# Kernel optimization log

Measured on AMD Instinct MI355X. Metric: run time of the kernel, lower is better.

The kernel has to match this reference:

```python
import jax, jax.numpy as jnp
import numpy as np

N, M, D = 1024, 1024, 256

def setup_inputs() -> dict:
    key = jax.random.key(0)
    ks = jax.random.split(key, 10)
    s = 1.0 / np.sqrt(D)
    return {
        "f_r": jax.random.normal(ks[0], (N, D), jnp.float32),
        "f_r_prime": jax.random.normal(ks[1], (M, D), jnp.float32),
        "W_w": jax.random.uniform(ks[2], (D, D), jnp.float32, -s, s),
        "W_b": jax.random.uniform(ks[3], (D,), jnp.float32, -s, s),
        "Wp_w": jax.random.uniform(ks[4], (D, D), jnp.float32, -s, s),
        "Wp_b": jax.random.uniform(ks[5], (D,), jnp.float32, -s, s),
        "w_w": jax.random.uniform(ks[6], (1, D), jnp.float32, -s, s),
        "w_b": jax.random.uniform(ks[7], (1,), jnp.float32, -s, s),
        "wp_w": jax.random.uniform(ks[8], (1, D), jnp.float32, -s, s),
        "wp_b": jax.random.uniform(ks[9], (1,), jnp.float32, -s, s),
    }

def reference(f_r, f_r_prime, W_w, W_b, Wp_w, Wp_b, w_w, w_b, wp_w, wp_b):
    q = f_r @ W_w.T + W_b            # [N, D]
    k = f_r_prime @ Wp_w.T + Wp_b    # [M, D]
    # additive (Bahdanau) scores: tanh over broadcast sum [N, M, D]
    h = jnp.tanh(q[:, None, :] + k[None, :, :])
    alpha = h @ w_w.T + w_b          # [N, M, 1]
    alpha = jax.nn.softmax(alpha, axis=1)
    # stage-1 pooling over M (weights on raw f_r_prime, as in source)
    context = jnp.sum(alpha * f_r_prime[None, :, :], axis=1)  # [N, D]
    # stage-2 attention pooling over N
    alpha_p = jax.nn.softmax(context @ wp_w.T + wp_b, axis=0)  # [N, 1]
    pool = jnp.sum(alpha_p * context, axis=0, keepdims=True)   # [1, D]
    return pool
```

## Files before the change

kernel.cpp:

```cpp
#include <hip/hip_runtime.h>

#define NN 1024
#define MM 1024
#define DD 256

__device__ __forceinline__ float rcp_fast(float x) { return __builtin_amdgcn_rcpf(x); }

__global__ __launch_bounds__(256) void gemm_exp_kernel(
    const float* __restrict__ f_r,  const float* __restrict__ W_w,  const float* __restrict__ W_b,
    const float* __restrict__ f_rp, const float* __restrict__ Wp_w, const float* __restrict__ Wp_b,
    float* __restrict__ Eq, float* __restrict__ EkT, float* __restrict__ out0)
{
    const int b    = blockIdx.x;
    const int mat  = b >> 7;
    const int tile = b & 127;
    const int rt = tile & 31, dt = tile >> 5;
    const float* __restrict__ A    = mat ? f_rp : f_r;
    const float* __restrict__ B    = mat ? Wp_w : W_w;
    const float* __restrict__ bias = mat ? Wp_b : W_b;

    __shared__ float As[32][36];
    __shared__ float Bs[32][68];
    __shared__ float T[64][36];

    const int t  = threadIdx.x;
    if (b == 0) out0[t] = 0.f;
    const int tx = t & 15, ty = t >> 4;
    const int r0 = rt * 32, d0 = dt * 64;
    const int ar = t >> 3, ak = (t & 7) * 4;
    const int br = t >> 2, bk = (t & 3) * 8;

    float acc[2][4];
    #pragma unroll
    for (int i = 0; i < 2; ++i)
        #pragma unroll
        for (int j = 0; j < 4; ++j) acc[i][j] = 0.f;

    for (int kk = 0; kk < DD; kk += 32) {
        float4 av  = *(const float4*)(A + (size_t)(r0 + ar) * DD + kk + ak);
        float4 bv0 = *(const float4*)(B + (size_t)(d0 + br) * DD + kk + bk);
        float4 bv1 = *(const float4*)(B + (size_t)(d0 + br) * DD + kk + bk + 4);
        __syncthreads();
        As[ak + 0][ar] = av.x; As[ak + 1][ar] = av.y; As[ak + 2][ar] = av.z; As[ak + 3][ar] = av.w;
        Bs[bk + 0][br] = bv0.x; Bs[bk + 1][br] = bv0.y; Bs[bk + 2][br] = bv0.z; Bs[bk + 3][br] = bv0.w;
        Bs[bk + 4][br] = bv1.x; Bs[bk + 5][br] = bv1.y; Bs[bk + 6][br] = bv1.z; Bs[bk + 7][br] = bv1.w;
        __syncthreads();
        #pragma unroll
        for (int k = 0; k < 32; ++k) {
            float2 a2 = *(const float2*)&As[k][ty * 2];
            float4 b4 = *(const float4*)&Bs[k][tx * 4];
            float aa[2] = {a2.x, a2.y};
            float bb[4] = {b4.x, b4.y, b4.z, b4.w};
            #pragma unroll
            for (int i = 0; i < 2; ++i)
                #pragma unroll
                for (int j = 0; j < 4; ++j)
                    acc[i][j] = fmaf(aa[i], bb[j], acc[i][j]);
        }
    }

    float bj[4];
    #pragma unroll
    for (int j = 0; j < 4; ++j) bj[j] = bias[d0 + tx * 4 + j];

    float e[2][4];
    #pragma unroll
    for (int i = 0; i < 2; ++i)
        #pragma unroll
        for (int j = 0; j < 4; ++j) {
            float v = acc[i][j] + bj[j];
            v = fminf(fmaxf(v, -10.f), 10.f);
            e[i][j] = __expf(2.f * v);
        }

    if (mat == 0) {
        #pragma unroll
        for (int i = 0; i < 2; ++i)
            *(float4*)&Eq[(size_t)(r0 + ty * 2 + i) * DD + d0 + tx * 4] =
                make_float4(e[i][0], e[i][1], e[i][2], e[i][3]);
    } else {
        __syncthreads();
        #pragma unroll
        for (int i = 0; i < 2; ++i)
            #pragma unroll
            for (int j = 0; j < 4; ++j) T[tx * 4 + j][ty * 2 + i] = e[i][j];
        __syncthreads();
        const int dl = t >> 3, rl = (t & 7) * 4;
        #pragma unroll
        for (int h = 0; h < 2; ++h) {
            int dloc = dl + 32 * h;
            float4 tv = *(const float4*)&T[dloc][rl];
            *(float4*)&EkT[(size_t)(d0 + dloc) * MM + r0 + rl] = tv;
        }
    }
}

__global__ __launch_bounds__(512, 8) void score_softmax_kernel(
    const float* __restrict__ Eq, const float* __restrict__ EkT,
    const float* __restrict__ w_w, float* __restrict__ alpha)
{
    __shared__ float eq[2 * DD];
    __shared__ float w2[DD];
    __shared__ float accbuf[8][256];
    __shared__ float redmx[8 * 2];
    __shared__ float redsm[8 * 2];

    const int t  = threadIdx.x;
    const int tg = t >> 8;
    const int tm = t & 255;
    const int lane = t & 63, wid = t >> 6;
    const int n0 = blockIdx.x * 2;
    const int dh = tg * 128;

    eq[t] = Eq[(size_t)n0 * DD + t];
    if (t < DD) w2[t] = -2.0f * w_w[t];
    __syncthreads();

    float acc[2][4];
    #pragma unroll
    for (int n = 0; n < 2; ++n)
        #pragma unroll
        for (int j = 0; j < 4; ++j) acc[n][j] = 0.f;

    const float* ekb = EkT + (size_t)dh * MM + 4 * tm;

    for (int g = 0; g < 32; ++g) {
        const int db = g * 4;
        float4 k0 = *(const float4*)(ekb + (size_t)(db + 0) * MM);
        float4 k1 = *(const float4*)(ekb + (size_t)(db + 1) * MM);
        float4 k2 = *(const float4*)(ekb + (size_t)(db + 2) * MM);
        float4 k3 = *(const float4*)(ekb + (size_t)(db + 3) * MM);
        float4 w4 = *(const float4*)&w2[dh + db];
        float4 qA = *(const float4*)&eq[dh + db];
        float4 qB = *(const float4*)&eq[DD + dh + db];

        float ka[2][4] = {{k0.x, k0.y, k0.z, k0.w}, {k2.x, k2.y, k2.z, k2.w}};
        float kb[2][4] = {{k1.x, k1.y, k1.z, k1.w}, {k3.x, k3.y, k3.z, k3.w}};
        float wa[2] = {w4.x, w4.z}, wb[2] = {w4.y, w4.w};
        float qa[2][2] = {{qA.x, qA.z}, {qB.x, qB.z}};
        float qb[2][2] = {{qA.y, qA.w}, {qB.y, qB.w}};

        #pragma unroll
        for (int pp = 0; pp < 2; ++pp)
            #pragma unroll
            for (int n = 0; n < 2; ++n)
                #pragma unroll
                for (int j = 0; j < 4; ++j) {
                    float x0 = fmaf(qa[n][pp], ka[pp][j], 1.f);
                    float x1 = fmaf(qb[n][pp], kb[pp][j], 1.f);
                    float p  = x0 * x1;
                    float tn = fmaf(wb[pp], x0, wa[pp] * x1);
                    acc[n][j] = fmaf(tn, rcp_fast(p), acc[n][j]);
                }
    }

    if (tg == 1) {
        #pragma unroll
        for (int n = 0; n < 2; ++n)
            #pragma unroll
            for (int j = 0; j < 4; ++j) accbuf[n * 4 + j][tm] = acc[n][j];
    }
    __syncthreads();
    if (tg == 0) {
        #pragma unroll
        for (int n = 0; n < 2; ++n)
            #pragma unroll
            for (int j = 0; j < 4; ++j) acc[n][j] += accbuf[n * 4 + j][tm];
    }

    float mx[2];
    #pragma unroll
    for (int n = 0; n < 2; ++n) {
        mx[n] = (tg == 0) ? fmaxf(fmaxf(acc[n][0], acc[n][1]), fmaxf(acc[n][2], acc[n][3])) : -3e38f;
        #pragma unroll
        for (int off = 32; off > 0; off >>= 1) mx[n] = fmaxf(mx[n], __shfl_xor(mx[n], off));
    }
    if (lane == 0) { redmx[wid * 2] = mx[0]; redmx[wid * 2 + 1] = mx[1]; }
    __syncthreads();
    float MX[2];
    #pragma unroll
    for (int n = 0; n < 2; ++n) {
        float m = redmx[n];
        #pragma unroll
        for (int w = 1; w < 8; ++w) m = fmaxf(m, redmx[w * 2 + n]);
        MX[n] = m;
    }

    float e[2][4], sm[2];
    #pragma unroll
    for (int n = 0; n < 2; ++n) {
        sm[n] = 0.f;
        #pragma unroll
        for (int j = 0; j < 4; ++j) {
            e[n][j] = (tg == 0) ? __expf(acc[n][j] - MX[n]) : 0.f;
            sm[n] += e[n][j];
        }
        #pragma unroll
        for (int off = 32; off > 0; off >>= 1) sm[n] += __shfl_xor(sm[n], off);
    }
    if (lane == 0) { redsm[wid * 2] = sm[0]; redsm[wid * 2 + 1] = sm[1]; }
    __syncthreads();
    if (tg == 0) {
        #pragma unroll
        for (int n = 0; n < 2; ++n) {
            float s = redsm[n];
            #pragma unroll
            for (int w = 1; w < 8; ++w) s += redsm[w * 2 + n];
            float inv = rcp_fast(s);
            *(float4*)&alpha[(size_t)(n0 + n) * MM + 4 * tm] =
                make_float4(e[n][0] * inv, e[n][1] * inv, e[n][2] * inv, e[n][3] * inv);
        }
    }
}

__global__ __launch_bounds__(256) void context_kernel(
    const float* __restrict__ alpha, const float* __restrict__ frp,
    float* __restrict__ part)
{
    __shared__ float als[16][128];
    const int t  = threadIdx.x;
    const int bm = blockIdx.x & 7;
    const int bn = blockIdx.x >> 3;
    const int dq = t & 63;
    const int ng = t >> 6;

    #pragma unroll
    for (int i = 0; i < 2; ++i) {
        int f4i = t + i * 256;
        int row = f4i >> 5, c4 = f4i & 31;
        *(float4*)&als[row][c4 * 4] =
            *(const float4*)&alpha[(size_t)(bn * 16 + row) * MM + bm * 128 + c4 * 4];
    }
    __syncthreads();

    float acc[4][4];
    #pragma unroll
    for (int n = 0; n < 4; ++n)
        #pragma unroll
        for (int j = 0; j < 4; ++j) acc[n][j] = 0.f;

    const float* fb = frp + (size_t)(bm * 128) * DD + 4 * dq;
    for (int m4 = 0; m4 < 32; ++m4) {
        float av[4][4];
        #pragma unroll
        for (int n = 0; n < 4; ++n) {
            float4 a4 = *(const float4*)&als[ng * 4 + n][m4 * 4];
            av[n][0] = a4.x; av[n][1] = a4.y; av[n][2] = a4.z; av[n][3] = a4.w;
        }
        #pragma unroll
        for (int mm = 0; mm < 4; ++mm) {
            float4 f4 = *(const float4*)(fb + (size_t)(m4 * 4 + mm) * DD);
            float fv[4] = {f4.x, f4.y, f4.z, f4.w};
            #pragma unroll
            for (int n = 0; n < 4; ++n)
                #pragma unroll
                for (int j = 0; j < 4; ++j)
                    acc[n][j] = fmaf(av[n][mm], fv[j], acc[n][j]);
        }
    }
    #pragma unroll
    for (int n = 0; n < 4; ++n)
        *(float4*)&part[((size_t)bm << 18) + (size_t)(bn * 16 + ng * 4 + n) * DD + 4 * dq] =
            make_float4(acc[n][0], acc[n][1], acc[n][2], acc[n][3]);
}

__global__ __launch_bounds__(256) void ctx_reduce_kernel(
    const float* __restrict__ part, const float* __restrict__ wp_w,
    float* __restrict__ ctx, float* __restrict__ score)
{
    __shared__ float red[4];
    const int t = threadIdx.x;
    const int n = blockIdx.x;
    const int lane = t & 63, wid = t >> 6;
    size_t idx = (size_t)n * DD + t;
    float c = 0.f;
    #pragma unroll
    for (int s = 0; s < 8; ++s) c += part[idx + ((size_t)s << 18)];
    ctx[idx] = c;
    float p = c * wp_w[t];
    #pragma unroll
    for (int off = 32; off > 0; off >>= 1) p += __shfl_xor(p, off);
    if (lane == 0) red[wid] = p;
    __syncthreads();
    if (t == 0) score[n] = red[0] + red[1] + red[2] + red[3];
}

__global__ __launch_bounds__(256) void pool_kernel(
    const float* __restrict__ ctx, const float* __restrict__ score,
    float* __restrict__ out)
{
    __shared__ float red[8];
    __shared__ float wloc[16];
    const int t = threadIdx.x, lane = t & 63, wid = t >> 6;

    float s0 = score[t], s1 = score[t + 256], s2 = score[t + 512], s3 = score[t + 768];
    float mx = fmaxf(fmaxf(s0, s1), fmaxf(s2, s3));
    #pragma unroll
    for (int off = 32; off > 0; off >>= 1) mx = fmaxf(mx, __shfl_xor(mx, off));
    if (lane == 0) red[wid] = mx;
    __syncthreads();
    mx = fmaxf(fmaxf(red[0], red[1]), fmaxf(red[2], red[3]));

    float se = __expf(s0 - mx) + __expf(s1 - mx) + __expf(s2 - mx) + __expf(s3 - mx);
    #pragma unroll
    for (int off = 32; off > 0; off >>= 1) se += __shfl_xor(se, off);
    if (lane == 0) red[4 + wid] = se;
    __syncthreads();
    se = red[4] + red[5] + red[6] + red[7];
    float invS = rcp_fast(se);

    if (t < 16) wloc[t] = __expf(score[blockIdx.x * 16 + t] - mx) * invS;
    __syncthreads();

    float pool = 0.f;
    const float* cb = ctx + (size_t)(blockIdx.x * 16) * DD + t;
    #pragma unroll
    for (int i = 0; i < 16; ++i) pool = fmaf(wloc[i], cb[i * DD], pool);
    atomicAdd(out + t, pool);
}

extern "C" void kernel_launch(void* const* d_in, const int* in_sizes, int n_in,
                              void* d_out, int out_size, void* d_ws, size_t ws_size,
                              hipStream_t stream) {
    const float* f_r  = (const float*)d_in[0];
    const float* f_rp = (const float*)d_in[1];
    const float* W_w  = (const float*)d_in[2];
    const float* W_b  = (const float*)d_in[3];
    const float* Wp_w = (const float*)d_in[4];
    const float* Wp_b = (const float*)d_in[5];
    const float* w_w  = (const float*)d_in[6];
    const float* wp_w = (const float*)d_in[8];
    float* out = (float*)d_out;

    float* ws    = (float*)d_ws;
    float* Eq    = ws;
    float* EkT   = ws + 262144;
    float* alpha = ws + 524288;
    float* part  = ws + 1572864;
    float* ctx   = ws + 3670016;
    float* score = ws + 3932160;

    gemm_exp_kernel<<<256, 256, 0, stream>>>(f_r, W_w, W_b, f_rp, Wp_w, Wp_b, Eq, EkT, out);
    score_softmax_kernel<<<512, 512, 0, stream>>>(Eq, EkT, w_w, alpha);
    context_kernel<<<512, 256, 0, stream>>>(alpha, f_rp, part);
    ctx_reduce_kernel<<<1024, 256, 0, stream>>>(part, wp_w, ctx, score);
    pool_kernel<<<64, 256, 0, stream>>>(ctx, score, out);
}
```

Before: 135.3 us.

## Pack score loop into float2 ops, prefetch EkT, fuse pool into reduce

Result: slower. 223.2 us (+65.0%).

```diff
diff --git a/kernel.cpp b/kernel.cpp
--- a/kernel.cpp
+++ b/kernel.cpp
@@ -4,12 +4,14 @@
 #define MM 1024
 #define DD 256
 
+typedef float floatx2 __attribute__((ext_vector_type(2)));
+
 __device__ __forceinline__ float rcp_fast(float x) { return __builtin_amdgcn_rcpf(x); }
 
 __global__ __launch_bounds__(256) void gemm_exp_kernel(
     const float* __restrict__ f_r,  const float* __restrict__ W_w,  const float* __restrict__ W_b,
     const float* __restrict__ f_rp, const float* __restrict__ Wp_w, const float* __restrict__ Wp_b,
-    float* __restrict__ Eq, float* __restrict__ EkT, float* __restrict__ out0)
+    float* __restrict__ Eq, float* __restrict__ EkT, unsigned int* __restrict__ cnt)
 {
     const int b    = blockIdx.x;
     const int mat  = b >> 7;
@@ -24,7 +26,7 @@
     __shared__ float T[64][36];
 
     const int t  = threadIdx.x;
-    if (b == 0) out0[t] = 0.f;
+    if (b == 0 && t == 0) *cnt = 0;
     const int tx = t & 15, ty = t >> 4;
     const int r0 = rt * 32, d0 = dt * 64;
     const int ar = t >> 3, ak = (t & 7) * 4;
@@ -95,7 +97,7 @@
     }
 }
 
-__global__ __launch_bounds__(512, 8) void score_softmax_kernel(
+__global__ __launch_bounds__(512, 4) void score_softmax_kernel(
     const float* __restrict__ Eq, const float* __restrict__ EkT,
     const float* __restrict__ w_w, float* __restrict__ alpha)
 {
@@ -116,42 +118,69 @@
     if (t < DD) w2[t] = -2.0f * w_w[t];
     __syncthreads();
 
-    float acc[2][4];
-    #pragma unroll
-    for (int n = 0; n < 2; ++n)
-        #pragma unroll
-        for (int j = 0; j < 4; ++j) acc[n][j] = 0.f;
+    const floatx2 one2 = {1.f, 1.f};
+    floatx2 accl[2] = {{0.f, 0.f}, {0.f, 0.f}};
+    floatx2 acch[2] = {{0.f, 0.f}, {0.f, 0.f}};
 
     const float* ekb = EkT + (size_t)dh * MM + 4 * tm;
 
+    float4 c0 = *(const float4*)(ekb + 0 * MM);
+    float4 c1 = *(const float4*)(ekb + 1 * MM);
+    float4 c2 = *(const float4*)(ekb + 2 * MM);
+    float4 c3 = *(const float4*)(ekb + 3 * MM);
+
     for (int g = 0; g < 32; ++g) {
+        float4 p0, p1, p2, p3;
+        if (g < 31) {
+            const float* nb = ekb + (size_t)(g * 4 + 4) * MM;
+            p0 = *(const float4*)(nb + 0 * MM);
+            p1 = *(const float4*)(nb + 1 * MM);
+            p2 = *(const float4*)(nb + 2 * MM);
+            p3 = *(const float4*)(nb + 3 * MM);
+        }
         const int db = g * 4;
-        float4 k0 = *(const float4*)(ekb + (size_t)(db + 0) * MM);
-        float4 k1 = *(const float4*)(ekb + (size_t)(db + 1) * MM);
-        float4 k2 = *(const float4*)(ekb + (size_t)(db + 2) * MM);
-        float4 k3 = *(const float4*)(ekb + (size_t)(db + 3) * MM);
         float4 w4 = *(const float4*)&w2[dh + db];
         float4 qA = *(const float4*)&eq[dh + db];
         float4 qB = *(const float4*)&eq[DD + dh + db];
 
-        float ka[2][4] = {{k0.x, k0.y, k0.z, k0.w}, {k2.x, k2.y, k2.z, k2.w}};
-        float kb[2][4] = {{k1.x, k1.y, k1.z, k1.w}, {k3.x, k3.y, k3.z, k3.w}};
-        float wa[2] = {w4.x, w4.z}, wb[2] = {w4.y, w4.w};
-        float qa[2][2] = {{qA.x, qA.z}, {qB.x, qB.z}};
-        float qb[2][2] = {{qA.y, qA.w}, {qB.y, qB.w}};
-
-        #pragma unroll
-        for (int pp = 0; pp < 2; ++pp)
-            #pragma unroll
-            for (int n = 0; n < 2; ++n)
-                #pragma unroll
-                for (int j = 0; j < 4; ++j) {
-                    float x0 = fmaf(qa[n][pp], ka[pp][j], 1.f);
-                    float x1 = fmaf(qb[n][pp], kb[pp][j], 1.f);
-                    float p  = x0 * x1;
-                    float tn = fmaf(wb[pp], x0, wa[pp] * x1);
-                    acc[n][j] = fmaf(tn, rcp_fast(p), acc[n][j]);
-                }
+        floatx2 k0l = {c0.x, c0.y}, k0h = {c0.z, c0.w};
+        floatx2 k1l = {c1.x, c1.y}, k1h = {c1.z, c1.w};
+        floatx2 k2l = {c2.x, c2.y}, k2h = {c2.z, c2.w};
+        floatx2 k3l = {c3.x, c3.y}, k3h = {c3.z, c3.w};
+        floatx2 wa0 = {w4.x, w4.x}, wb0 = {w4.y, w4.y};
+        floatx2 wa1 = {w4.z, w4.z}, wb1 = {w4.w, w4.w};
+        float qs[2][4] = {{qA.x, qA.y, qA.z, qA.w}, {qB.x, qB.y, qB.z, qB.w}};
+
+        #pragma unroll
+        for (int n = 0; n < 2; ++n) {
+            floatx2 qa0 = {qs[n][0], qs[n][0]}, qb0 = {qs[n][1], qs[n][1]};
+            floatx2 qa1 = {qs[n][2], qs[n][2]}, qb1 = {qs[n][3], qs[n][3]};
+            floatx2 x0 = qa0 * k0l + one2, x1 = qb0 * k1l + one2;
+            floatx2 pr = x0 * x1;
+            floatx2 tn = wa0 * x1 + wb0 * x0;
+            floatx2 r;  r.x = rcp_fast(pr.x);  r.y = rcp_fast(pr.y);
+            accl[n] += tn * r;
+            x0 = qa0 * k0h + one2; x1 = qb0 * k1h + one2;
+            pr = x0 * x1; tn = wa0 * x1 + wb0 * x0;
+            r.x = rcp_fast(pr.x);  r.y = rcp_fast(pr.y);
+            acch[n] += tn * r;
+            x0 = qa1 * k2l + one2; x1 = qb1 * k3l + one2;
+            pr = x0 * x1; tn = wa1 * x1 + wb1 * x0;
+            r.x = rcp_fast(pr.x);  r.y = rcp_fast(pr.y);
+            accl[n] += tn * r;
+            x0 = qa1 * k2h + one2; x1 = qb1 * k3h + one2;
+            pr = x0 * x1; tn = wa1 * x1 + wb1 * x0;
+            r.x = rcp_fast(pr.x);  r.y = rcp_fast(pr.y);
+            acch[n] += tn * r;
+        }
+        c0 = p0; c1 = p1; c2 = p2; c3 = p3;
+    }
+
+    float acc[2][4];
+    #pragma unroll
+    for (int n = 0; n < 2; ++n) {
+        acc[n][0] = accl[n].x; acc[n][1] = accl[n].y;
+        acc[n][2] = acch[n].x; acc[n][3] = acch[n].y;
     }
 
     if (tg == 1) {
@@ -264,59 +293,72 @@
             make_float4(acc[n][0], acc[n][1], acc[n][2], acc[n][3]);
 }
 
-__global__ __launch_bounds__(256) void ctx_reduce_kernel(
+__global__ __launch_bounds__(256) void reduce_pool_kernel(
     const float* __restrict__ part, const float* __restrict__ wp_w,
-    float* __restrict__ ctx, float* __restrict__ score)
+    float* __restrict__ ctx, float* __restrict__ score,
+    unsigned int* __restrict__ cnt, float* __restrict__ out)
 {
     __shared__ float red[4];
+    __shared__ float red2[8];
+    __shared__ float wl[1024];
+    __shared__ int lastFlag;
+
     const int t = threadIdx.x;
     const int n = blockIdx.x;
     const int lane = t & 63, wid = t >> 6;
+
     size_t idx = (size_t)n * DD + t;
     float c = 0.f;
     #pragma unroll
     for (int s = 0; s < 8; ++s) c += part[idx + ((size_t)s << 18)];
     ctx[idx] = c;
+
     float p = c * wp_w[t];
     #pragma unroll
     for (int off = 32; off > 0; off >>= 1) p += __shfl_xor(p, off);
     if (lane == 0) red[wid] = p;
     __syncthreads();
     if (t == 0) score[n] = red[0] + red[1] + red[2] + red[3];
-}
-
-__global__ __launch_bounds__(256) void pool_kernel(
-    const float* __restrict__ ctx, const float* __restrict__ score,
-    float* __restrict__ out)
-{
-    __shared__ float red[8];
-    __shared__ float wloc[16];
-    const int t = threadIdx.x, lane = t & 63, wid = t >> 6;
+
+    __threadfence();
+    __syncthreads();
+    if (t == 0) {
+        unsigned int old = atomicAdd(cnt, 1u);
+        lastFlag = (old == gridDim.x - 1);
+    }
+    __syncthreads();
+    if (!lastFlag) return;
+    __threadfence();
 
     float s0 = score[t], s1 = score[t + 256], s2 = score[t + 512], s3 = score[t + 768];
     float mx = fmaxf(fmaxf(s0, s1), fmaxf(s2, s3));
     #pragma unroll
     for (int off = 32; off > 0; off >>= 1) mx = fmaxf(mx, __shfl_xor(mx, off));
-    if (lane == 0) red[wid] = mx;
-    __syncthreads();
-    mx = fmaxf(fmaxf(red[0], red[1]), fmaxf(red[2], red[3]));
-
-    float se = __expf(s0 - mx) + __expf(s1 - mx) + __expf(s2 - mx) + __expf(s3 - mx);
+    if (lane == 0) red2[wid] = mx;
+    __syncthreads();
+    mx = fmaxf(fmaxf(red2[0], red2[1]), fmaxf(red2[2], red2[3]));
+
+    float e0 = __expf(s0 - mx), e1 = __expf(s1 - mx), e2 = __expf(s2 - mx), e3 = __expf(s3 - mx);
+    float se = e0 + e1 + e2 + e3;
     #pragma unroll
     for (int off = 32; off > 0; off >>= 1) se += __shfl_xor(se, off);
-    if (lane == 0) red[4 + wid] = se;
-    __syncthreads();
-    se = red[4] + red[5] + red[6] + red[7];
+    if (lane == 0) red2[4 + wid] = se;
+    __syncthreads();
+    se = red2[4] + red2[5] + red2[6] + red2[7];
     float invS = rcp_fast(se);
 
-    if (t < 16) wloc[t] = __expf(score[blockIdx.x * 16 + t] - mx) * invS;
-    __syncthreads();
-
-    float pool = 0.f;
-    const float* cb = ctx + (size_t)(blockIdx.x * 16) * DD + t;
-    #pragma unroll
-    for (int i = 0; i < 16; ++i) pool = fmaf(wloc[i], cb[i * DD], pool);
-    atomicAdd(out + t, pool);
+    wl[t] = e0 * invS; wl[t + 256] = e1 * invS; wl[t + 512] = e2 * invS; wl[t + 768] = e3 * invS;
+    __syncthreads();
+
+    float a0 = 0.f, a1 = 0.f, a2 = 0.f, a3 = 0.f;
+    #pragma unroll 4
+    for (int nn = 0; nn < 256; ++nn) {
+        a0 = fmaf(wl[nn],       ctx[(size_t)nn * DD + t],          a0);
+        a1 = fmaf(wl[nn + 256], ctx[(size_t)(nn + 256) * DD + t],  a1);
+        a2 = fmaf(wl[nn + 512], ctx[(size_t)(nn + 512) * DD + t],  a2);
+        a3 = fmaf(wl[nn + 768], ctx[(size_t)(nn + 768) * DD + t],  a3);
+    }
+    out[t] = (a0 + a1) + (a2 + a3);
 }
 
 extern "C" void kernel_launch(void* const* d_in, const int* in_sizes, int n_in,
@@ -339,10 +381,10 @@
     float* part  = ws + 1572864;
     float* ctx   = ws + 3670016;
     float* score = ws + 3932160;
-
-    gemm_exp_kernel<<<256, 256, 0, stream>>>(f_r, W_w, W_b, f_rp, Wp_w, Wp_b, Eq, EkT, out);
+    unsigned int* cnt = (unsigned int*)(ws + 3933184);
+
+    gemm_exp_kernel<<<256, 256, 0, stream>>>(f_r, W_w, W_b, f_rp, Wp_w, Wp_b, Eq, EkT, cnt);
     score_softmax_kernel<<<512, 512, 0, stream>>>(Eq, EkT, w_w, alpha);
     context_kernel<<<512, 256, 0, stream>>>(alpha, f_rp, part);
-    ctx_reduce_kernel<<<1024, 256, 0, stream>>>(part, wp_w, ctx, score);
-    pool_kernel<<<64, 256, 0, stream>>>(ctx, score, out);
-}
+    reduce_pool_kernel<<<1024, 256, 0, stream>>>(part, wp_w, ctx, score, cnt, out);
+}
```
